# Kernel tuning notes

Hardware: AMD Instinct MI355X
Metric: run time of the kernel (lower is better)

Reference implementation:

```python
import jax, jax.numpy as jnp
import numpy as np

NUM_HEADS = 16
SOFTPLUS_EPS = 1e-4


def rotate_half(x):
    x1, x2 = jnp.split(x, 2, axis=-1)
    return jnp.concatenate((-x2, x1), axis=-1)


def setup_inputs() -> dict:
    key = jax.random.key(0)
    B, S, H = 1, 2048, 2048
    D = H // NUM_HEADS  # 128
    ks = jax.random.split(key, 5)
    hidden_states = jax.random.normal(ks[0], (B, S, H), dtype=jnp.float32)
    # standard RoPE tables: [S, D]
    inv_freq = 1.0 / (10000.0 ** (np.arange(0, D, 2, dtype=np.float32) / D))
    freqs = np.outer(np.arange(S, dtype=np.float32), inv_freq)  # [S, D/2]
    emb = np.concatenate([freqs, freqs], axis=-1)  # [S, D]
    cos = jnp.asarray(np.cos(emb), dtype=jnp.float32)
    sin = jnp.asarray(np.sin(emb), dtype=jnp.float32)
    std = 0.02
    w_q = jax.random.normal(ks[1], (2 * H, H), dtype=jnp.float32) * std
    w_k = jax.random.normal(ks[2], (2 * H, H), dtype=jnp.float32) * std
    w_v = jax.random.normal(ks[3], (H, H), dtype=jnp.float32) * std
    w_o = jax.random.normal(ks[4], (H, H), dtype=jnp.float32) * std
    return {"hidden_states": hidden_states, "cos": cos, "sin": sin,
            "w_q": w_q, "w_k": w_k, "w_v": w_v, "w_o": w_o}


def reference(hidden_states, cos, sin, w_q, w_k, w_v, w_o):
    B, S, H = hidden_states.shape
    NH = NUM_HEADS
    D = H // NH
    # projections (torch Linear: y = x @ W.T)
    q = (hidden_states @ w_q.T).reshape(B, S, NH, 2 * D).swapaxes(1, 2)  # [B,NH,S,2D]
    k = (hidden_states @ w_k.T).reshape(B, S, NH, 2 * D).swapaxes(1, 2)
    v = (hidden_states @ w_v.T).reshape(B, S, NH, D).swapaxes(1, 2)      # [B,NH,S,D]
    q_mu, q_sigma_raw = jnp.split(q, 2, axis=-1)
    k_mu, k_sigma_raw = jnp.split(k, 2, axis=-1)
    q_sigma = jax.nn.softplus(q_sigma_raw) + SOFTPLUS_EPS
    k_sigma = jax.nn.softplus(k_sigma_raw) + SOFTPLUS_EPS
    q_w = q_mu / jnp.sqrt(q_sigma)
    k_w = k_mu / jnp.sqrt(k_sigma)
    # RoPE on variance-weighted means; cos/sin [S,D] broadcast over [B,NH,S,D]
    q_w = q_w * cos + rotate_half(q_w) * sin
    k_w = k_w * cos + rotate_half(k_w) * sin
    q_sq = jnp.sum(q_w * q_w, axis=-1, keepdims=True)          # [B,NH,S,1]
    k_sq = jnp.sum(k_w * k_w, axis=-1, keepdims=True)          # [B,NH,S,1]
    dot = jnp.einsum('bhqd,bhkd->bhqk', q_w, k_w)              # [B,NH,S,S]
    weighted_dist = q_sq + jnp.swapaxes(k_sq, -2, -1) - 2.0 * dot
    log_det_q = jnp.sum(jnp.log(q_sigma), axis=-1, keepdims=True)
    log_det_k = jnp.sum(jnp.log(k_sigma), axis=-1, keepdims=True)
    log_det = log_det_q + jnp.swapaxes(log_det_k, -2, -1)
    attn_scores = -0.5 * (weighted_dist + log_det)
    attn_probs = jax.nn.softmax(attn_scores, axis=-1)
    attn_out = jnp.einsum('bhqk,bhkd->bhqd', attn_probs, v)    # [B,NH,S,D]
    attn_out = attn_out.swapaxes(1, 2).reshape(B, S, H)
    return attn_out @ w_o.T
```

## Files before the change

### kernel.cpp

```cpp
#include <hip/hip_runtime.h>
#include <stdint.h>

#define S_LEN 2048
#define HID   2048
#define NHEAD 16
#define HD    128
#define NQK   8192
#define K_HID 2048

typedef _Float16 f16x8 __attribute__((ext_vector_type(8)));
typedef float    f32x4 __attribute__((ext_vector_type(4)));

__device__ __forceinline__ unsigned short f2h(float f) {
    _Float16 h = (_Float16)f;
    union { _Float16 h; unsigned short u; } c; c.h = h;
    return c.u;
}
__device__ __forceinline__ float h2f(unsigned short b) {
    union { unsigned short u; _Float16 h; } c; c.u = b;
    return (float)c.h;
}
__device__ __forceinline__ float softplus_f(float x) {
    return (x > 20.f) ? x : log1pf(expf(x));
}
__device__ __forceinline__ unsigned pk2h(float a, float b) {
    auto w = __builtin_amdgcn_cvt_pkrtz(a, b);
    union { decltype(w) h; unsigned u; } c; c.h = w;
    return c.u;
}
#define EXP2F(x) __builtin_amdgcn_exp2f(x)
#define LOG2E 1.44269504088896f
__device__ __forceinline__ void gload_lds16(const unsigned short* g, unsigned short* l) {
    __builtin_amdgcn_global_load_lds(
        (const __attribute__((address_space(1))) unsigned int*)g,
        (__attribute__((address_space(3))) unsigned int*)l, 16, 0, 0);
}
__device__ __forceinline__ void bar() {
    asm volatile("" ::: "memory");
    __builtin_amdgcn_s_barrier();
    asm volatile("" ::: "memory");
}
#define VMCNT(n) asm volatile("s_waitcnt vmcnt(" #n ")" ::: "memory")

__global__ __launch_bounds__(256) void cast5(const float* __restrict__ hs,
                                             const float* __restrict__ wq,
                                             const float* __restrict__ wk,
                                             const float* __restrict__ wv,
                                             const float* __restrict__ wo,
                                             unsigned short* __restrict__ hs16,
                                             unsigned short* __restrict__ wqk16,
                                             unsigned short* __restrict__ wv16,
                                             unsigned short* __restrict__ wo16) {
    int b = blockIdx.x;
    const float* src;
    unsigned short* dst;
    int i;
    if (b < 4096)       { src = hs; dst = hs16;                          i = b; }
    else if (b < 12288) { src = wq; dst = wqk16;                         i = b - 4096; }
    else if (b < 20480) { src = wk; dst = wqk16 + (size_t)4096 * K_HID;  i = b - 12288; }
    else if (b < 24576) { src = wv; dst = wv16;                          i = b - 20480; }
    else                { src = wo; dst = wo16;                          i = b - 24576; }
    int idx = i * 256 + threadIdx.x;
    float4 v = ((const float4*)src)[idx];
    ushort4 o;
    o.x = f2h(v.x); o.y = f2h(v.y); o.z = f2h(v.z); o.w = f2h(v.w);
    ((ushort4*)dst)[idx] = o;
}

template <bool OUT_F16>
__device__ __forceinline__ void gemm_body(const unsigned short* __restrict__ A,
                                          const unsigned short* __restrict__ B,
                                          void* __restrict__ Cv,
                                          int m0, int n0, int N,
                                          unsigned short* As, unsigned short* Bs) {
    const int t    = threadIdx.x;
    const int wave = t >> 6;
    const int lane = t & 63;
    const int wm   = wave >> 1, wn = wave & 1;
    const int lrow = lane & 15, quad = lane >> 4;
    const int srow = lane >> 2;
    const int scol = (lane & 3) * 8;

    f32x4 acc[4][4];
    for (int i = 0; i < 4; ++i)
        for (int j = 0; j < 4; ++j)
            acc[i][j] = (f32x4){0.f, 0.f, 0.f, 0.f};

    for (int k0 = 0; k0 < K_HID; k0 += 32) {
        for (int c = 0; c < 2; ++c) {
            int ch = wave * 2 + c;
            int row = ch * 16 + srow;
            gload_lds16(A + (size_t)(m0 + row) * K_HID + k0 + scol, &As[ch * 512]);
            gload_lds16(B + (size_t)(n0 + row) * K_HID + k0 + scol, &Bs[ch * 512]);
        }
        __syncthreads();

        f16x8 af[4], bfr[4];
        for (int tm = 0; tm < 4; ++tm)
            af[tm]  = *(const f16x8*)(&As[(wm * 64 + tm * 16 + lrow) * 32 + quad * 8]);
        for (int tn = 0; tn < 4; ++tn)
            bfr[tn] = *(const f16x8*)(&Bs[(wn * 64 + tn * 16 + lrow) * 32 + quad * 8]);
        for (int tm = 0; tm < 4; ++tm)
            for (int tn = 0; tn < 4; ++tn)
                acc[tm][tn] = __builtin_amdgcn_mfma_f32_16x16x32_f16(af[tm], bfr[tn], acc[tm][tn], 0, 0, 0);
        __syncthreads();
    }

    for (int tm = 0; tm < 4; ++tm)
        for (int tn = 0; tn < 4; ++tn) {
            int col = n0 + wn * 64 + tn * 16 + lrow;
            for (int r = 0; r < 4; ++r) {
                int row = m0 + wm * 64 + tm * 16 + quad * 4 + r;
                if (OUT_F16)
                    ((unsigned short*)Cv)[(size_t)row * N + col] = f2h(acc[tm][tn][r]);
                else
                    ((float*)Cv)[(size_t)row * N + col] = acc[tm][tn][r];
            }
        }
}

__global__ __launch_bounds__(256) void gemm_qkv(const unsigned short* __restrict__ hs16,
                                                const unsigned short* __restrict__ wqk16,
                                                const unsigned short* __restrict__ wv16,
                                                unsigned short* __restrict__ qk16,
                                                unsigned short* __restrict__ Vt) {
    __shared__ __align__(16) unsigned short As[128 * 32];
    __shared__ __align__(16) unsigned short Bs[128 * 32];
    int b = blockIdx.x;
    if (b < 1024) {
        gemm_body<true>(hs16, wqk16, qk16, (b >> 6) * 128, (b & 63) * 128, NQK, As, Bs);
    } else {
        b -= 1024;
        gemm_body<true>(wv16, hs16, Vt, (b >> 4) * 128, (b & 15) * 128, S_LEN, As, Bs);
    }
}

template <bool OUT_F16>
__global__ __launch_bounds__(256) void gemm_nt_f16(const unsigned short* __restrict__ A,
                                                   const unsigned short* __restrict__ B,
                                                   void* __restrict__ Cv,
                                                   int M, int N, int Kd) {
    __shared__ __align__(16) unsigned short As[128 * 32];
    __shared__ __align__(16) unsigned short Bs[128 * 32];
    gemm_body<OUT_F16>(A, B, Cv, blockIdx.y * 128, blockIdx.x * 128, N, As, Bs);
}

__global__ __launch_bounds__(512, 2) void gemm256_qk(const unsigned short* __restrict__ A,
                                                     const unsigned short* __restrict__ B,
                                                     unsigned short* __restrict__ C) {
    extern __shared__ __align__(16) unsigned short lds[];
    const int t    = threadIdx.x;
    const int wave = t >> 6;
    const int lane = t & 63;
    const int wm   = wave >> 2, wn = wave & 3;
    const int lrow = lane & 15, quad = lane >> 4;

    const int x  = blockIdx.x & 7;
    const int sl = blockIdx.x >> 3;
    const int tm = ((x >> 2) << 2) + (sl >> 3);
    const int tn = ((x & 3) << 3) + (sl & 7);
    const int m0 = tm << 8, n0 = tn << 8;

    const int srow = lane >> 2;
    const int scol = ((lane & 3) * 8) ^ ((lane >> 5) << 4);
    const unsigned short* Ag = A + (size_t)(m0 + wave * 16 + srow) * K_HID + scol;
    const unsigned short* Bg = B + (size_t)(n0 + wave * 16 + srow) * K_HID + scol;

    const int swz = (lrow * 32 + quad * 8) ^ ((lrow >> 3) << 4);

    f32x4 acc[8][4];
    #pragma unroll
    for (int i = 0; i < 8; ++i)
        #pragma unroll
        for (int j = 0; j < 4; ++j) acc[i][j] = (f32x4){0.f, 0.f, 0.f, 0.f};

    {
        unsigned short* la = lds + wave * 1024;
        gload_lds16(Ag,               la);
        gload_lds16(Ag + 32,          la + 512);
        gload_lds16(Ag + 262144,      la + 8192);
        gload_lds16(Ag + 262144 + 32, la + 8704);
        unsigned short* lb = la + 16384;
        gload_lds16(Bg,               lb);
        gload_lds16(Bg + 32,          lb + 512);
        gload_lds16(Bg + 262144,      lb + 8192);
        gload_lds16(Bg + 262144 + 32, lb + 8704);
    }
    VMCNT(0);
    bar();

    f16x8 ah[4][2], b01[2][2];

    const int NT = K_HID / 64;
    #pragma unroll 1
    for (int t2 = 0; t2 < NT; ++t2) {
        const int buf = t2 & 1;
        const unsigned short* Lb = lds + buf * 32768;
        unsigned short*       Ln = lds + (buf ^ 1) * 32768 + wave * 1024;
        const int k1  = (t2 + 1) * 64;
        const bool pre = (t2 < NT - 1);

        f16x8 al[4][2], b23[2][2];

        if (pre) {
            gload_lds16(Ag + k1,               Ln);
            gload_lds16(Ag + k1 + 32,          Ln + 512);
            gload_lds16(Ag + 262144 + k1,      Ln + 8192);
            gload_lds16(Ag + 262144 + k1 + 32, Ln + 8704);
        }
        #pragma unroll
        for (int i = 0; i < 4; ++i) {
            al[i][0] = *(const f16x8*)(Lb + (wm * 8 + i) * 1024 + swz);
            al[i][1] = *(const f16x8*)(Lb + (wm * 8 + i) * 1024 + 512 + swz);
        }
        if (t2) {
            __builtin_amdgcn_s_setprio(1);
            #pragma unroll
            for (int i = 0; i < 4; ++i)
                #pragma unroll
                for (int j = 0; j < 2; ++j) {
                    acc[4 + i][j] = __builtin_amdgcn_mfma_f32_16x16x32_f16(ah[i][0], b01[j][0], acc[4 + i][j], 0, 0, 0);
                    acc[4 + i][j] = __builtin_amdgcn_mfma_f32_16x16x32_f16(ah[i][1], b01[j][1], acc[4 + i][j], 0, 0, 0);
                }
            __builtin_amdgcn_s_setprio(0);
        }
        #pragma unroll
        for (int j = 0; j < 2; ++j) {
            b01[j][0] = *(const f16x8*)(Lb + 16384 + (wn * 4 + j) * 1024 + swz);
            b01[j][1] = *(const f16x8*)(Lb + 16384 + (wn * 4 + j) * 1024 + 512 + swz);
        }
        bar();

        if (pre) {
            gload_lds16(Bg + k1,               Ln + 16384);
            gload_lds16(Bg + k1 + 32,          Ln + 16896);
            gload_lds16(Bg + 262144 + k1,      Ln + 24576);
            gload_lds16(Bg + 262144 + k1 + 32, Ln + 25088);
        }
        #pragma unroll
        for (int j = 0; j < 2; ++j) {
            b23[j][0] = *(const f16x8*)(Lb + 16384 + (wn * 4 + 2 + j) * 1024 + swz);
            b23[j][1] = *(const f16x8*)(Lb + 16384 + (wn * 4 + 2 + j) * 1024 + 512 + swz);
        }
        __builtin_amdgcn_s_setprio(1);
        #pragma unroll
        for (int i = 0; i < 4; ++i)
            #pragma unroll
            for (int j = 0; j < 2; ++j) {
                acc[i][j] = __builtin_amdgcn_mfma_f32_16x16x32_f16(al[i][0], b01[j][0], acc[i][j], 0, 0, 0);
                acc[i][j] = __builtin_amdgcn_mfma_f32_16x16x32_f16(al[i][1], b01[j][1], acc[i][j], 0, 0, 0);
            }
        __builtin_amdgcn_s_setprio(0);
        bar();

        #pragma unroll
        for (int i = 0; i < 4; ++i) {
            ah[i][0] = *(const f16x8*)(Lb + (wm * 8 + 4 + i) * 1024 + swz);
            ah[i][1] = *(const f16x8*)(Lb + (wm * 8 + 4 + i) * 1024 + 512 + swz);
        }
        __builtin_amdgcn_s_setprio(1);
        #pragma unroll
        for (int i = 0; i < 4; ++i)
            #pragma unroll
            for (int j = 0; j < 2; ++j) {
                acc[i][2 + j] = __builtin_amdgcn_mfma_f32_16x16x32_f16(al[i][0], b23[j][0], acc[i][2 + j], 0, 0, 0);
                acc[i][2 + j] = __builtin_amdgcn_mfma_f32_16x16x32_f16(al[i][1], b23[j][1], acc[i][2 + j], 0, 0, 0);
            }
        __builtin_amdgcn_s_setprio(0);
        bar();

        __builtin_amdgcn_s_setprio(1);
        #pragma unroll
        for (int i = 0; i < 4; ++i)
            #pragma unroll
            for (int j = 0; j < 2; ++j) {
                acc[4 + i][2 + j] = __builtin_amdgcn_mfma_f32_16x16x32_f16(ah[i][0], b23[j][0], acc[4 + i][2 + j], 0, 0, 0);
                acc[4 + i][2 + j] = __builtin_amdgcn_mfma_f32_16x16x32_f16(ah[i][1], b23[j][1], acc[4 + i][2 + j], 0, 0, 0);
            }
        __builtin_amdgcn_s_setprio(0);
        VMCNT(0);
        bar();
    }

    __builtin_amdgcn_s_setprio(1);
    #pragma unroll
    for (int i = 0; i < 4; ++i)
        #pragma unroll
        for (int j = 0; j < 2; ++j) {
            acc[4 + i][j] = __builtin_amdgcn_mfma_f32_16x16x32_f16(ah[i][0], b01[j][0], acc[4 + i][j], 0, 0, 0);
            acc[4 + i][j] = __builtin_amdgcn_mfma_f32_16x16x32_f16(ah[i][1], b01[j][1], acc[4 + i][j], 0, 0, 0);
        }
    __builtin_amdgcn_s_setprio(0);

    #pragma unroll
    for (int m = 0; m < 8; ++m)
        #pragma unroll
        for (int n = 0; n < 4; ++n) {
            const int col = n0 + wn * 64 + n * 16 + lrow;
            #pragma unroll
            for (int r = 0; r < 4; ++r) {
                const int row = m0 + wm * 128 + m * 16 + quad * 4 + r;
                C[(size_t)row * NQK + col] = f2h(acc[m][n][r]);
            }
        }
}

__global__ __launch_bounds__(256) void prep_qk(const unsigned short* __restrict__ qk,
                                               const float* __restrict__ cosb,
                                               const float* __restrict__ sinb,
                                               unsigned short* __restrict__ Q16,
                                               unsigned short* __restrict__ K16,
                                               float* __restrict__ kbias) {
    int gid  = blockIdx.x * 4 + (threadIdx.x >> 6);
    int lane = threadIdx.x & 63;
    int h = gid >> 11;
    int s = gid & 2047;
    int d1 = lane, d2 = lane + 64;
    const unsigned short* row = qk + (size_t)s * NQK;
    float c1 = cosb[s * HD + d1], c2 = cosb[s * HD + d2];
    float s1 = sinb[s * HD + d1], s2 = sinb[s * HD + d2];
    size_t ob = ((size_t)h * S_LEN + s) * HD;

    {
        int base = h * 256;
        float mu1 = h2f(row[base + d1]),       mu2 = h2f(row[base + d2]);
        float sg1 = softplus_f(h2f(row[base + 128 + d1])) + 1e-4f;
        float sg2 = softplus_f(h2f(row[base + 128 + d2])) + 1e-4f;
        float w1 = mu1 * rsqrtf(sg1), w2 = mu2 * rsqrtf(sg2);
        float o1 = w1 * c1 - w2 * s1;
        float o2 = w2 * c2 + w1 * s2;
        Q16[ob + d1] = f2h(o1 * LOG2E);
        Q16[ob + d2] = f2h(o2 * LOG2E);
    }
    {
        int base = 4096 + h * 256;
        float mu1 = h2f(row[base + d1]),       mu2 = h2f(row[base + d2]);
        float sg1 = softplus_f(h2f(row[base + 128 + d1])) + 1e-4f;
        float sg2 = softplus_f(h2f(row[base + 128 + d2])) + 1e-4f;
        float w1 = mu1 * rsqrtf(sg1), w2 = mu2 * rsqrtf(sg2);
        float o1 = w1 * c1 - w2 * s1;
        float o2 = w2 * c2 + w1 * s2;
        unsigned short k1 = f2h(o1), k2 = f2h(o2);
        K16[ob + d1] = k1; K16[ob + d2] = k2;
        float r1 = h2f(k1), r2 = h2f(k2);
        float part = r1 * r1 + r2 * r2 + logf(sg1) + logf(sg2);
        for (int off = 32; off > 0; off >>= 1) part += __shfl_down(part, off);
        if (lane == 0) kbias[(size_t)h * S_LEN + s] = -0.5f * LOG2E * part;
    }
}

__global__ __launch_bounds__(256, 2) void flash_mfma(const unsigned short* __restrict__ Q16,
                                                     const unsigned short* __restrict__ K16,
                                                     const unsigned short* __restrict__ Vt,
                                                     const float* __restrict__ kbias,
                                                     unsigned short* __restrict__ OP,
                                                     float* __restrict__ ML) {
    constexpr int LV = 72;
    __shared__ __align__(16) unsigned short Khs[4 * 64 * 32];
    __shared__ __align__(16) unsigned short Vts[2 * 128 * 32];
    __shared__ __align__(16) unsigned short Ps[128 * LV];
    __shared__ float kb[64];

    const int t    = threadIdx.x;
    const int bb   = blockIdx.x;
    const int cc   = (bb & 7) | (((bb >> 7) & 3) << 3);
    const int h    = cc & 15;
    const int kz   = cc >> 4;
    const int q0   = ((bb >> 3) & 15) * 128;
    const int wave = t >> 6;
    const int lane = t & 63;
    const int lrow = lane & 15, quad = lane >> 4;
    const int srow = lane >> 2;
    const int scol = (lane & 3) * 8;

    f16x8 qf[2][4];
    for (int m = 0; m < 2; ++m) {
        size_t rb = ((size_t)h * S_LEN + q0 + wave * 32 + m * 16 + lrow) * HD;
        for (int kk = 0; kk < 4; ++kk)
            qf[m][kk] = *(const f16x8*)(Q16 + rb + kk * 32 + quad * 8);
    }

    float mrow[2], lsum[2];
    f32x4 Ofr[2][8];
    for (int m = 0; m < 2; ++m) { mrow[m] = -INFINITY; lsum[m] = 0.f; }
    for (int m = 0; m < 2; ++m)
        for (int d = 0; d < 8; ++d) Ofr[m][d] = (f32x4){0.f, 0.f, 0.f, 0.f};

    const int kbeg = kz * 1024;
    for (int k0 = kbeg; k0 < kbeg + 1024; k0 += 64) {
        {
            const unsigned short* kgb = K16 + ((size_t)h * S_LEN + k0) * HD;
            const unsigned short* vgb = Vt + ((size_t)h * HD) * S_LEN + k0;
            for (int c = 0; c < 4; ++c) {
                int ch = wave * 4 + c;
                int kk = ch >> 2;
                int r  = (ch & 3) * 16 + srow;
                gload_lds16(kgb + (size_t)r * HD + kk * 32 + scol, &Khs[ch * 512]);
                int kc = ch >> 3;
                int r2 = (ch & 7) * 16 + srow;
                gload_lds16(vgb + (size_t)r2 * S_LEN + kc * 32 + scol, &Vts[ch * 512]);
            }
            if (t < 64) kb[t] = kbias[(size_t)h * S_LEN + k0 + t];
        }
        __syncthreads();

        f32x4 sc[2][4];
        for (int m = 0; m < 2; ++m)
            for (int nt = 0; nt < 4; ++nt) sc[m][nt] = (f32x4){0.f, 0.f, 0.f, 0.f};
        for (int kk = 0; kk < 4; ++kk)
            for (int nt = 0; nt < 4; ++nt) {
                f16x8 khf = *(const f16x8*)(&Khs[kk * 2048 + (nt * 16 + lrow) * 32 + quad * 8]);
                sc[0][nt] = __builtin_amdgcn_mfma_f32_16x16x32_f16(khf, qf[0][kk], sc[0][nt], 0, 0, 0);
                sc[1][nt] = __builtin_amdgcn_mfma_f32_16x16x32_f16(khf, qf[1][kk], sc[1][nt], 0, 0, 0);
            }

        f32x4 kbv[4];
        #pragma unroll
        for (int nt = 0; nt < 4; ++nt)
            kbv[nt] = *(const f32x4*)(&kb[nt * 16 + quad * 4]);

        #pragma unroll
        for (int m = 0; m < 2; ++m) {
            float s[4][4];
            float mx = -INFINITY;
            #pragma unroll
            for (int nt = 0; nt < 4; ++nt)
                #pragma unroll
                for (int r = 0; r < 4; ++r) {
                    s[nt][r] = sc[m][nt][r] + kbv[nt][r];
                    mx = fmaxf(mx, s[nt][r]);
                }
            mx = fmaxf(mx, __shfl_xor(mx, 16));
            mx = fmaxf(mx, __shfl_xor(mx, 32));
            float mnew  = fmaxf(mrow[m], mx);
            float alpha = EXP2F(mrow[m] - mnew);
            mrow[m] = mnew;
            float psum = 0.f;
            unsigned pw[8];
            #pragma unroll
            for (int nt = 0; nt < 4; ++nt) {
                float p0 = EXP2F(s[nt][0] - mnew);
                float p1 = EXP2F(s[nt][1] - mnew);
                float p2 = EXP2F(s[nt][2] - mnew);
                float p3 = EXP2F(s[nt][3] - mnew);
                psum += (p0 + p1) + (p2 + p3);
                pw[nt * 2]     = pk2h(p0, p1);
                pw[nt * 2 + 1] = pk2h(p2, p3);
            }
            lsum[m] = lsum[m] * alpha + psum;
            float av0 = __shfl(alpha, quad * 4 + 0);
            float av1 = __shfl(alpha, quad * 4 + 1);
            float av2 = __shfl(alpha, quad * 4 + 2);
            float av3 = __shfl(alpha, quad * 4 + 3);
            #pragma unroll
            for (int dt = 0; dt < 8; ++dt) {
                Ofr[m][dt][0] *= av0;
                Ofr[m][dt][1] *= av1;
                Ofr[m][dt][2] *= av2;
                Ofr[m][dt][3] *= av3;
            }
            int prow = (wave * 32 + m * 16 + lrow) * LV;
            #pragma unroll
            for (int nt = 0; nt < 4; ++nt) {
                uint2 wv; wv.x = pw[nt * 2]; wv.y = pw[nt * 2 + 1];
                *(uint2*)(&Ps[prow + nt * 16 + quad * 4]) = wv;
            }
        }

        for (int c = 0; c < 2; ++c) {
            f16x8 pa0 = *(const f16x8*)(&Ps[(wave * 32 + lrow) * LV + c * 32 + quad * 8]);
            f16x8 pa1 = *(const f16x8*)(&Ps[(wave * 32 + 16 + lrow) * LV + c * 32 + quad * 8]);
            for (int dt = 0; dt < 8; ++dt) {
                f16x8 vb = *(const f16x8*)(&Vts[c * 4096 + (dt * 16 + lrow) * 32 + quad * 8]);
                Ofr[0][dt] = __builtin_amdgcn_mfma_f32_16x16x32_f16(pa0, vb, Ofr[0][dt], 0, 0, 0);
                Ofr[1][dt] = __builtin_amdgcn_mfma_f32_16x16x32_f16(pa1, vb, Ofr[1][dt], 0, 0, 0);
            }
        }
        __syncthreads();
    }

    size_t obase = (size_t)(kz * NHEAD + h) * S_LEN;
    for (int m = 0; m < 2; ++m) {
        float rs = lsum[m];
        rs += __shfl_xor(rs, 16);
        rs += __shfl_xor(rs, 32);
        if (quad == 0) {
            int qrow = q0 + wave * 32 + m * 16 + lrow;
            ML[(obase + qrow) * 2]     = mrow[m];
            ML[(obase + qrow) * 2 + 1] = rs;
        }
        for (int r = 0; r < 4; ++r) {
            int qrow = q0 + wave * 32 + m * 16 + quad * 4 + r;
            unsigned short* op = OP + (obase + qrow) * HD;
            for (int dt = 0; dt < 8; ++dt)
                op[dt * 16 + lrow] = f2h(Ofr[m][dt][r]);
        }
    }
}

__global__ __launch_bounds__(256) void flash_merge(const unsigned short* __restrict__ OP,
                                                   const float* __restrict__ ML,
                                                   unsigned short* __restrict__ Obf) {
    int row = blockIdx.x * 2 + (threadIdx.x >> 7);
    int d   = threadIdx.x & 127;
    int h = row >> 11, q = row & 2047;
    size_t i0 = (size_t)h * S_LEN + q;
    size_t i1 = (size_t)(NHEAD + h) * S_LEN + q;
    float m0 = ML[i0 * 2], l0 = ML[i0 * 2 + 1];
    float m1 = ML[i1 * 2], l1 = ML[i1 * 2 + 1];
    float mf = fmaxf(m0, m1);
    float w0 = EXP2F(m0 - mf), w1 = EXP2F(m1 - mf);
    float inv = 1.f / (l0 * w0 + l1 * w1);
    float o = (h2f(OP[i0 * HD + d]) * w0 + h2f(OP[i1 * HD + d]) * w1) * inv;
    Obf[(size_t)q * HID + h * HD + d] = f2h(o);
}

extern "C" void kernel_launch(void* const* d_in, const int* in_sizes, int n_in,
                              void* d_out, int out_size, void* d_ws, size_t ws_size,
                              hipStream_t stream) {
    const float* hs   = (const float*)d_in[0];
    const float* cosb = (const float*)d_in[1];
    const float* sinb = (const float*)d_in[2];
    const float* wq   = (const float*)d_in[3];
    const float* wk   = (const float*)d_in[4];
    const float* wv   = (const float*)d_in[5];
    const float* wo   = (const float*)d_in[6];
    float* out = (float*)d_out;
    char*  ws  = (char*)d_ws;

    unsigned short* w_qk16 = (unsigned short*)(ws);
    unsigned short* Q16    = (unsigned short*)(ws);
    unsigned short* K16    = (unsigned short*)(ws + 8388608);
    float*          kbias  = (float*)(ws + 16777216);
    unsigned short* qk16   = (unsigned short*)(ws + 33554432);
    unsigned short* OP     = (unsigned short*)(ws + 33554432);
    float*          ML     = (float*)(ws + 50331648);
    unsigned short* hs16   = (unsigned short*)(ws + 67108864);
    unsigned short* Obf    = (unsigned short*)(ws + 67108864);
    unsigned short* w_v16  = (unsigned short*)(ws + 75497472);
    unsigned short* w_o16  = (unsigned short*)(ws + 83886080);
    unsigned short* Vt     = (unsigned short*)(ws + 92274688);

    static int use256 = -1;
    if (use256 < 0) {
        hipError_t e = hipFuncSetAttribute((const void*)gemm256_qk,
                                           hipFuncAttributeMaxDynamicSharedMemorySize,
                                           131072);
        use256 = (e == hipSuccess) ? 1 : 0;
    }

    cast5<<<28672, 256, 0, stream>>>(hs, wq, wk, wv, wo, hs16, w_qk16, w_v16, w_o16);

    if (use256) {
        gemm256_qk<<<256, 512, 131072, stream>>>(hs16, w_qk16, qk16);
        gemm_nt_f16<true><<<dim3(16, 16), 256, 0, stream>>>(w_v16, hs16, Vt, HID, S_LEN, K_HID);
    } else {
        gemm_qkv<<<1280, 256, 0, stream>>>(hs16, w_qk16, w_v16, qk16, Vt);
    }

    prep_qk<<<(NHEAD * S_LEN) / 4, 256, 0, stream>>>(qk16, cosb, sinb,
                                                     Q16, K16, kbias);
    flash_mfma<<<512, 256, 0, stream>>>(Q16, K16, Vt, kbias, OP, ML);
    flash_merge<<<(NHEAD * S_LEN) / 2, 256, 0, stream>>>(OP, ML, Obf);
    gemm_nt_f16<false><<<dim3(16, 16), 256, 0, stream>>>(Obf, w_o16, out, S_LEN, HID, K_HID);
}
```

Measured before the change: 379.6 us.

## Fuse V projection with QK prep kernel and skip redundant softmax rescales

The V projection GEMM and the per-row Q/K prep (softplus, RoPE, key bias) now run as one launch, with separate block ranges doing each job. This removes a kernel boundary and lets the two independent workloads share the GPU. In the flash kernel the key bias is used as the initial MFMA accumulator, which removes a separate add. The running-max rescale of the output accumulators is skipped when no lane's row maximum increases, at the cost of a wave-wide vote and a branch per step.

```diff
diff --git a/kernel.cpp b/kernel.cpp
--- a/kernel.cpp
+++ b/kernel.cpp
@@ -119,200 +119,13 @@
         }
 }
 
-__global__ __launch_bounds__(256) void gemm_qkv(const unsigned short* __restrict__ hs16,
-                                                const unsigned short* __restrict__ wqk16,
-                                                const unsigned short* __restrict__ wv16,
-                                                unsigned short* __restrict__ qk16,
-                                                unsigned short* __restrict__ Vt) {
-    __shared__ __align__(16) unsigned short As[128 * 32];
-    __shared__ __align__(16) unsigned short Bs[128 * 32];
-    int b = blockIdx.x;
-    if (b < 1024) {
-        gemm_body<true>(hs16, wqk16, qk16, (b >> 6) * 128, (b & 63) * 128, NQK, As, Bs);
-    } else {
-        b -= 1024;
-        gemm_body<true>(wv16, hs16, Vt, (b >> 4) * 128, (b & 15) * 128, S_LEN, As, Bs);
-    }
-}
-
-template <bool OUT_F16>
-__global__ __launch_bounds__(256) void gemm_nt_f16(const unsigned short* __restrict__ A,
-                                                   const unsigned short* __restrict__ B,
-                                                   void* __restrict__ Cv,
-                                                   int M, int N, int Kd) {
-    __shared__ __align__(16) unsigned short As[128 * 32];
-    __shared__ __align__(16) unsigned short Bs[128 * 32];
-    gemm_body<OUT_F16>(A, B, Cv, blockIdx.y * 128, blockIdx.x * 128, N, As, Bs);
-}
-
-__global__ __launch_bounds__(512, 2) void gemm256_qk(const unsigned short* __restrict__ A,
-                                                     const unsigned short* __restrict__ B,
-                                                     unsigned short* __restrict__ C) {
-    extern __shared__ __align__(16) unsigned short lds[];
-    const int t    = threadIdx.x;
-    const int wave = t >> 6;
-    const int lane = t & 63;
-    const int wm   = wave >> 2, wn = wave & 3;
-    const int lrow = lane & 15, quad = lane >> 4;
-
-    const int x  = blockIdx.x & 7;
-    const int sl = blockIdx.x >> 3;
-    const int tm = ((x >> 2) << 2) + (sl >> 3);
-    const int tn = ((x & 3) << 3) + (sl & 7);
-    const int m0 = tm << 8, n0 = tn << 8;
-
-    const int srow = lane >> 2;
-    const int scol = ((lane & 3) * 8) ^ ((lane >> 5) << 4);
-    const unsigned short* Ag = A + (size_t)(m0 + wave * 16 + srow) * K_HID + scol;
-    const unsigned short* Bg = B + (size_t)(n0 + wave * 16 + srow) * K_HID + scol;
-
-    const int swz = (lrow * 32 + quad * 8) ^ ((lrow >> 3) << 4);
-
-    f32x4 acc[8][4];
-    #pragma unroll
-    for (int i = 0; i < 8; ++i)
-        #pragma unroll
-        for (int j = 0; j < 4; ++j) acc[i][j] = (f32x4){0.f, 0.f, 0.f, 0.f};
-
-    {
-        unsigned short* la = lds + wave * 1024;
-        gload_lds16(Ag,               la);
-        gload_lds16(Ag + 32,          la + 512);
-        gload_lds16(Ag + 262144,      la + 8192);
-        gload_lds16(Ag + 262144 + 32, la + 8704);
-        unsigned short* lb = la + 16384;
-        gload_lds16(Bg,               lb);
-        gload_lds16(Bg + 32,          lb + 512);
-        gload_lds16(Bg + 262144,      lb + 8192);
-        gload_lds16(Bg + 262144 + 32, lb + 8704);
-    }
-    VMCNT(0);
-    bar();
-
-    f16x8 ah[4][2], b01[2][2];
-
-    const int NT = K_HID / 64;
-    #pragma unroll 1
-    for (int t2 = 0; t2 < NT; ++t2) {
-        const int buf = t2 & 1;
-        const unsigned short* Lb = lds + buf * 32768;
-        unsigned short*       Ln = lds + (buf ^ 1) * 32768 + wave * 1024;
-        const int k1  = (t2 + 1) * 64;
-        const bool pre = (t2 < NT - 1);
-
-        f16x8 al[4][2], b23[2][2];
-
-        if (pre) {
-            gload_lds16(Ag + k1,               Ln);
-            gload_lds16(Ag + k1 + 32,          Ln + 512);
-            gload_lds16(Ag + 262144 + k1,      Ln + 8192);
-            gload_lds16(Ag + 262144 + k1 + 32, Ln + 8704);
-        }
-        #pragma unroll
-        for (int i = 0; i < 4; ++i) {
-            al[i][0] = *(const f16x8*)(Lb + (wm * 8 + i) * 1024 + swz);
-            al[i][1] = *(const f16x8*)(Lb + (wm * 8 + i) * 1024 + 512 + swz);
-        }
-        if (t2) {
-            __builtin_amdgcn_s_setprio(1);
-            #pragma unroll
-            for (int i = 0; i < 4; ++i)
-                #pragma unroll
-                for (int j = 0; j < 2; ++j) {
-                    acc[4 + i][j] = __builtin_amdgcn_mfma_f32_16x16x32_f16(ah[i][0], b01[j][0], acc[4 + i][j], 0, 0, 0);
-                    acc[4 + i][j] = __builtin_amdgcn_mfma_f32_16x16x32_f16(ah[i][1], b01[j][1], acc[4 + i][j], 0, 0, 0);
-                }
-            __builtin_amdgcn_s_setprio(0);
-        }
-        #pragma unroll
-        for (int j = 0; j < 2; ++j) {
-            b01[j][0] = *(const f16x8*)(Lb + 16384 + (wn * 4 + j) * 1024 + swz);
-            b01[j][1] = *(const f16x8*)(Lb + 16384 + (wn * 4 + j) * 1024 + 512 + swz);
-        }
-        bar();
-
-        if (pre) {
-            gload_lds16(Bg + k1,               Ln + 16384);
-            gload_lds16(Bg + k1 + 32,          Ln + 16896);
-            gload_lds16(Bg + 262144 + k1,      Ln + 24576);
-            gload_lds16(Bg + 262144 + k1 + 32, Ln + 25088);
-        }
-        #pragma unroll
-        for (int j = 0; j < 2; ++j) {
-            b23[j][0] = *(const f16x8*)(Lb + 16384 + (wn * 4 + 2 + j) * 1024 + swz);
-            b23[j][1] = *(const f16x8*)(Lb + 16384 + (wn * 4 + 2 + j) * 1024 + 512 + swz);
-        }
-        __builtin_amdgcn_s_setprio(1);
-        #pragma unroll
-        for (int i = 0; i < 4; ++i)
-            #pragma unroll
-            for (int j = 0; j < 2; ++j) {
-                acc[i][j] = __builtin_amdgcn_mfma_f32_16x16x32_f16(al[i][0], b01[j][0], acc[i][j], 0, 0, 0);
-                acc[i][j] = __builtin_amdgcn_mfma_f32_16x16x32_f16(al[i][1], b01[j][1], acc[i][j], 0, 0, 0);
-            }
-        __builtin_amdgcn_s_setprio(0);
-        bar();
-
-        #pragma unroll
-        for (int i = 0; i < 4; ++i) {
-            ah[i][0] = *(const f16x8*)(Lb + (wm * 8 + 4 + i) * 1024 + swz);
-            ah[i][1] = *(const f16x8*)(Lb + (wm * 8 + 4 + i) * 1024 + 512 + swz);
-        }
-        __builtin_amdgcn_s_setprio(1);
-        #pragma unroll
-        for (int i = 0; i < 4; ++i)
-            #pragma unroll
-            for (int j = 0; j < 2; ++j) {
-                acc[i][2 + j] = __builtin_amdgcn_mfma_f32_16x16x32_f16(al[i][0], b23[j][0], acc[i][2 + j], 0, 0, 0);
-                acc[i][2 + j] = __builtin_amdgcn_mfma_f32_16x16x32_f16(al[i][1], b23[j][1], acc[i][2 + j], 0, 0, 0);
-            }
-        __builtin_amdgcn_s_setprio(0);
-        bar();
-
-        __builtin_amdgcn_s_setprio(1);
-        #pragma unroll
-        for (int i = 0; i < 4; ++i)
-            #pragma unroll
-            for (int j = 0; j < 2; ++j) {
-                acc[4 + i][2 + j] = __builtin_amdgcn_mfma_f32_16x16x32_f16(ah[i][0], b23[j][0], acc[4 + i][2 + j], 0, 0, 0);
-                acc[4 + i][2 + j] = __builtin_amdgcn_mfma_f32_16x16x32_f16(ah[i][1], b23[j][1], acc[4 + i][2 + j], 0, 0, 0);
-            }
-        __builtin_amdgcn_s_setprio(0);
-        VMCNT(0);
-        bar();
-    }
-
-    __builtin_amdgcn_s_setprio(1);
-    #pragma unroll
-    for (int i = 0; i < 4; ++i)
-        #pragma unroll
-        for (int j = 0; j < 2; ++j) {
-            acc[4 + i][j] = __builtin_amdgcn_mfma_f32_16x16x32_f16(ah[i][0], b01[j][0], acc[4 + i][j], 0, 0, 0);
-            acc[4 + i][j] = __builtin_amdgcn_mfma_f32_16x16x32_f16(ah[i][1], b01[j][1], acc[4 + i][j], 0, 0, 0);
-        }
-    __builtin_amdgcn_s_setprio(0);
-
-    #pragma unroll
-    for (int m = 0; m < 8; ++m)
-        #pragma unroll
-        for (int n = 0; n < 4; ++n) {
-            const int col = n0 + wn * 64 + n * 16 + lrow;
-            #pragma unroll
-            for (int r = 0; r < 4; ++r) {
-                const int row = m0 + wm * 128 + m * 16 + quad * 4 + r;
-                C[(size_t)row * NQK + col] = f2h(acc[m][n][r]);
-            }
-        }
-}
-
-__global__ __launch_bounds__(256) void prep_qk(const unsigned short* __restrict__ qk,
-                                               const float* __restrict__ cosb,
-                                               const float* __restrict__ sinb,
-                                               unsigned short* __restrict__ Q16,
-                                               unsigned short* __restrict__ K16,
-                                               float* __restrict__ kbias) {
-    int gid  = blockIdx.x * 4 + (threadIdx.x >> 6);
-    int lane = threadIdx.x & 63;
+__device__ __forceinline__ void prep_body(int gid, int lane,
+                                          const unsigned short* __restrict__ qk,
+                                          const float* __restrict__ cosb,
+                                          const float* __restrict__ sinb,
+                                          unsigned short* __restrict__ Q16,
+                                          unsigned short* __restrict__ K16,
+                                          float* __restrict__ kbias) {
     int h = gid >> 11;
     int s = gid & 2047;
     int d1 = lane, d2 = lane + 64;
@@ -349,6 +162,222 @@
     }
 }
 
+__global__ __launch_bounds__(256) void gemm_qkv(const unsigned short* __restrict__ hs16,
+                                                const unsigned short* __restrict__ wqk16,
+                                                const unsigned short* __restrict__ wv16,
+                                                unsigned short* __restrict__ qk16,
+                                                unsigned short* __restrict__ Vt) {
+    __shared__ __align__(16) unsigned short As[128 * 32];
+    __shared__ __align__(16) unsigned short Bs[128 * 32];
+    int b = blockIdx.x;
+    if (b < 1024) {
+        gemm_body<true>(hs16, wqk16, qk16, (b >> 6) * 128, (b & 63) * 128, NQK, As, Bs);
+    } else {
+        b -= 1024;
+        gemm_body<true>(wv16, hs16, Vt, (b >> 4) * 128, (b & 15) * 128, S_LEN, As, Bs);
+    }
+}
+
+template <bool OUT_F16>
+__global__ __launch_bounds__(256) void gemm_nt_f16(const unsigned short* __restrict__ A,
+                                                   const unsigned short* __restrict__ B,
+                                                   void* __restrict__ Cv,
+                                                   int M, int N, int Kd) {
+    __shared__ __align__(16) unsigned short As[128 * 32];
+    __shared__ __align__(16) unsigned short Bs[128 * 32];
+    gemm_body<OUT_F16>(A, B, Cv, blockIdx.y * 128, blockIdx.x * 128, N, As, Bs);
+}
+
+__global__ __launch_bounds__(256) void vt_prep(const unsigned short* __restrict__ wv16,
+                                               const unsigned short* __restrict__ hs16,
+                                               unsigned short* __restrict__ Vt,
+                                               const unsigned short* __restrict__ qk16,
+                                               const float* __restrict__ cosb,
+                                               const float* __restrict__ sinb,
+                                               unsigned short* __restrict__ Q16,
+                                               unsigned short* __restrict__ K16,
+                                               float* __restrict__ kbias) {
+    __shared__ __align__(16) unsigned short As[128 * 32];
+    __shared__ __align__(16) unsigned short Bs[128 * 32];
+    int b = blockIdx.x;
+    if (b < 256) {
+        gemm_body<true>(wv16, hs16, Vt, (b >> 4) * 128, (b & 15) * 128, S_LEN, As, Bs);
+    } else {
+        int gid = (b - 256) * 4 + (threadIdx.x >> 6);
+        prep_body(gid, threadIdx.x & 63, qk16, cosb, sinb, Q16, K16, kbias);
+    }
+}
+
+__global__ __launch_bounds__(256) void prep_qk(const unsigned short* __restrict__ qk,
+                                               const float* __restrict__ cosb,
+                                               const float* __restrict__ sinb,
+                                               unsigned short* __restrict__ Q16,
+                                               unsigned short* __restrict__ K16,
+                                               float* __restrict__ kbias) {
+    int gid = blockIdx.x * 4 + (threadIdx.x >> 6);
+    prep_body(gid, threadIdx.x & 63, qk, cosb, sinb, Q16, K16, kbias);
+}
+
+__global__ __launch_bounds__(512, 2) void gemm256_qk(const unsigned short* __restrict__ A,
+                                                     const unsigned short* __restrict__ B,
+                                                     unsigned short* __restrict__ C) {
+    extern __shared__ __align__(16) unsigned short lds[];
+    const int t    = threadIdx.x;
+    const int wave = t >> 6;
+    const int lane = t & 63;
+    const int wm   = wave >> 2, wn = wave & 3;
+    const int lrow = lane & 15, quad = lane >> 4;
+
+    const int x  = blockIdx.x & 7;
+    const int sl = blockIdx.x >> 3;
+    const int tm = ((x >> 2) << 2) + (sl >> 3);
+    const int tn = ((x & 3) << 3) + (sl & 7);
+    const int m0 = tm << 8, n0 = tn << 8;
+
+    const int srow = lane >> 2;
+    const int scol = ((lane & 3) * 8) ^ ((lane >> 5) << 4);
+    const unsigned short* Ag = A + (size_t)(m0 + wave * 16 + srow) * K_HID + scol;
+    const unsigned short* Bg = B + (size_t)(n0 + wave * 16 + srow) * K_HID + scol;
+
+    const int swz = (lrow * 32 + quad * 8) ^ ((lrow >> 3) << 4);
+
+    f32x4 acc[8][4];
+    #pragma unroll
+    for (int i = 0; i < 8; ++i)
+        #pragma unroll
+        for (int j = 0; j < 4; ++j) acc[i][j] = (f32x4){0.f, 0.f, 0.f, 0.f};
+
+    {
+        unsigned short* la = lds + wave * 1024;
+        gload_lds16(Ag,               la);
+        gload_lds16(Ag + 32,          la + 512);
+        gload_lds16(Ag + 262144,      la + 8192);
+        gload_lds16(Ag + 262144 + 32, la + 8704);
+        unsigned short* lb = la + 16384;
+        gload_lds16(Bg,               lb);
+        gload_lds16(Bg + 32,          lb + 512);
+        gload_lds16(Bg + 262144,      lb + 8192);
+        gload_lds16(Bg + 262144 + 32, lb + 8704);
+    }
+    VMCNT(0);
+    bar();
+
+    f16x8 ah[4][2], b01[2][2];
+
+    const int NT = K_HID / 64;
+    #pragma unroll 1
+    for (int t2 = 0; t2 < NT; ++t2) {
+        const int buf = t2 & 1;
+        const unsigned short* Lb = lds + buf * 32768;
+        unsigned short*       Ln = lds + (buf ^ 1) * 32768 + wave * 1024;
+        const int k1  = (t2 + 1) * 64;
+        const bool pre = (t2 < NT - 1);
+
+        f16x8 al[4][2], b23[2][2];
+
+        if (pre) {
+            gload_lds16(Ag + k1,               Ln);
+            gload_lds16(Ag + k1 + 32,          Ln + 512);
+            gload_lds16(Ag + 262144 + k1,      Ln + 8192);
+            gload_lds16(Ag + 262144 + k1 + 32, Ln + 8704);
+        }
+        #pragma unroll
+        for (int i = 0; i < 4; ++i) {
+            al[i][0] = *(const f16x8*)(Lb + (wm * 8 + i) * 1024 + swz);
+            al[i][1] = *(const f16x8*)(Lb + (wm * 8 + i) * 1024 + 512 + swz);
+        }
+        if (t2) {
+            __builtin_amdgcn_s_setprio(1);
+            #pragma unroll
+            for (int i = 0; i < 4; ++i)
+                #pragma unroll
+                for (int j = 0; j < 2; ++j) {
+                    acc[4 + i][j] = __builtin_amdgcn_mfma_f32_16x16x32_f16(ah[i][0], b01[j][0], acc[4 + i][j], 0, 0, 0);
+                    acc[4 + i][j] = __builtin_amdgcn_mfma_f32_16x16x32_f16(ah[i][1], b01[j][1], acc[4 + i][j], 0, 0, 0);
+                }
+            __builtin_amdgcn_s_setprio(0);
+        }
+        #pragma unroll
+        for (int j = 0; j < 2; ++j) {
+            b01[j][0] = *(const f16x8*)(Lb + 16384 + (wn * 4 + j) * 1024 + swz);
+            b01[j][1] = *(const f16x8*)(Lb + 16384 + (wn * 4 + j) * 1024 + 512 + swz);
+        }
+        bar();
+
+        if (pre) {
+            gload_lds16(Bg + k1,               Ln + 16384);
+            gload_lds16(Bg + k1 + 32,          Ln + 16896);
+            gload_lds16(Bg + 262144 + k1,      Ln + 24576);
+            gload_lds16(Bg + 262144 + k1 + 32, Ln + 25088);
+        }
+        #pragma unroll
+        for (int j = 0; j < 2; ++j) {
+            b23[j][0] = *(const f16x8*)(Lb + 16384 + (wn * 4 + 2 + j) * 1024 + swz);
+            b23[j][1] = *(const f16x8*)(Lb + 16384 + (wn * 4 + 2 + j) * 1024 + 512 + swz);
+        }
+        __builtin_amdgcn_s_setprio(1);
+        #pragma unroll
+        for (int i = 0; i < 4; ++i)
+            #pragma unroll
+            for (int j = 0; j < 2; ++j) {
+                acc[i][j] = __builtin_amdgcn_mfma_f32_16x16x32_f16(al[i][0], b01[j][0], acc[i][j], 0, 0, 0);
+                acc[i][j] = __builtin_amdgcn_mfma_f32_16x16x32_f16(al[i][1], b01[j][1], acc[i][j], 0, 0, 0);
+            }
+        __builtin_amdgcn_s_setprio(0);
+        bar();
+
+        #pragma unroll
+        for (int i = 0; i < 4; ++i) {
+            ah[i][0] = *(const f16x8*)(Lb + (wm * 8 + 4 + i) * 1024 + swz);
+            ah[i][1] = *(const f16x8*)(Lb + (wm * 8 + 4 + i) * 1024 + 512 + swz);
+        }
+        __builtin_amdgcn_s_setprio(1);
+        #pragma unroll
+        for (int i = 0; i < 4; ++i)
+            #pragma unroll
+            for (int j = 0; j < 2; ++j) {
+                acc[i][2 + j] = __builtin_amdgcn_mfma_f32_16x16x32_f16(al[i][0], b23[j][0], acc[i][2 + j], 0, 0, 0);
+                acc[i][2 + j] = __builtin_amdgcn_mfma_f32_16x16x32_f16(al[i][1], b23[j][1], acc[i][2 + j], 0, 0, 0);
+            }
+        __builtin_amdgcn_s_setprio(0);
+        bar();
+
+        __builtin_amdgcn_s_setprio(1);
+        #pragma unroll
+        for (int i = 0; i < 4; ++i)
+            #pragma unroll
+            for (int j = 0; j < 2; ++j) {
+                acc[4 + i][2 + j] = __builtin_amdgcn_mfma_f32_16x16x32_f16(ah[i][0], b23[j][0], acc[4 + i][2 + j], 0, 0, 0);
+                acc[4 + i][2 + j] = __builtin_amdgcn_mfma_f32_16x16x32_f16(ah[i][1], b23[j][1], acc[4 + i][2 + j], 0, 0, 0);
+            }
+        __builtin_amdgcn_s_setprio(0);
+        VMCNT(0);
+        bar();
+    }
+
+    __builtin_amdgcn_s_setprio(1);
+    #pragma unroll
+    for (int i = 0; i < 4; ++i)
+        #pragma unroll
+        for (int j = 0; j < 2; ++j) {
+            acc[4 + i][j] = __builtin_amdgcn_mfma_f32_16x16x32_f16(ah[i][0], b01[j][0], acc[4 + i][j], 0, 0, 0);
+            acc[4 + i][j] = __builtin_amdgcn_mfma_f32_16x16x32_f16(ah[i][1], b01[j][1], acc[4 + i][j], 0, 0, 0);
+        }
+    __builtin_amdgcn_s_setprio(0);
+
+    #pragma unroll
+    for (int m = 0; m < 8; ++m)
+        #pragma unroll
+        for (int n = 0; n < 4; ++n) {
+            const int col = n0 + wn * 64 + n * 16 + lrow;
+            #pragma unroll
+            for (int r = 0; r < 4; ++r) {
+                const int row = m0 + wm * 128 + m * 16 + quad * 4 + r;
+                C[(size_t)row * NQK + col] = f2h(acc[m][n][r]);
+            }
+        }
+}
+
 __global__ __launch_bounds__(256, 2) void flash_mfma(const unsigned short* __restrict__ Q16,
                                                      const unsigned short* __restrict__ K16,
                                                      const unsigned short* __restrict__ Vt,
@@ -404,9 +433,16 @@
         }
         __syncthreads();
 
+        f32x4 kbv[4];
+        #pragma unroll
+        for (int nt = 0; nt < 4; ++nt)
+            kbv[nt] = *(const f32x4*)(&kb[nt * 16 + quad * 4]);
+
         f32x4 sc[2][4];
+        #pragma unroll
         for (int m = 0; m < 2; ++m)
-            for (int nt = 0; nt < 4; ++nt) sc[m][nt] = (f32x4){0.f, 0.f, 0.f, 0.f};
+            #pragma unroll
+            for (int nt = 0; nt < 4; ++nt) sc[m][nt] = kbv[nt];
         for (int kk = 0; kk < 4; ++kk)
             for (int nt = 0; nt < 4; ++nt) {
                 f16x8 khf = *(const f16x8*)(&Khs[kk * 2048 + (nt * 16 + lrow) * 32 + quad * 8]);
@@ -414,51 +450,46 @@
                 sc[1][nt] = __builtin_amdgcn_mfma_f32_16x16x32_f16(khf, qf[1][kk], sc[1][nt], 0, 0, 0);
             }
 
-        f32x4 kbv[4];
-        #pragma unroll
-        for (int nt = 0; nt < 4; ++nt)
-            kbv[nt] = *(const f32x4*)(&kb[nt * 16 + quad * 4]);
-
         #pragma unroll
         for (int m = 0; m < 2; ++m) {
-            float s[4][4];
             float mx = -INFINITY;
             #pragma unroll
             for (int nt = 0; nt < 4; ++nt)
                 #pragma unroll
-                for (int r = 0; r < 4; ++r) {
-                    s[nt][r] = sc[m][nt][r] + kbv[nt][r];
-                    mx = fmaxf(mx, s[nt][r]);
-                }
+                for (int r = 0; r < 4; ++r)
+                    mx = fmaxf(mx, sc[m][nt][r]);
             mx = fmaxf(mx, __shfl_xor(mx, 16));
             mx = fmaxf(mx, __shfl_xor(mx, 32));
-            float mnew  = fmaxf(mrow[m], mx);
-            float alpha = EXP2F(mrow[m] - mnew);
-            mrow[m] = mnew;
+            if (!__all(mx <= mrow[m])) {
+                float mnew  = fmaxf(mrow[m], mx);
+                float alpha = EXP2F(mrow[m] - mnew);
+                mrow[m] = mnew;
+                lsum[m] *= alpha;
+                float av0 = __shfl(alpha, quad * 4 + 0);
+                float av1 = __shfl(alpha, quad * 4 + 1);
+                float av2 = __shfl(alpha, quad * 4 + 2);
+                float av3 = __shfl(alpha, quad * 4 + 3);
+                #pragma unroll
+                for (int dt = 0; dt < 8; ++dt) {
+                    Ofr[m][dt][0] *= av0;
+                    Ofr[m][dt][1] *= av1;
+                    Ofr[m][dt][2] *= av2;
+                    Ofr[m][dt][3] *= av3;
+                }
+            }
             float psum = 0.f;
             unsigned pw[8];
             #pragma unroll
             for (int nt = 0; nt < 4; ++nt) {
-                float p0 = EXP2F(s[nt][0] - mnew);
-                float p1 = EXP2F(s[nt][1] - mnew);
-                float p2 = EXP2F(s[nt][2] - mnew);
-                float p3 = EXP2F(s[nt][3] - mnew);
+                float p0 = EXP2F(sc[m][nt][0] - mrow[m]);
+                float p1 = EXP2F(sc[m][nt][1] - mrow[m]);
+                float p2 = EXP2F(sc[m][nt][2] - mrow[m]);
+                float p3 = EXP2F(sc[m][nt][3] - mrow[m]);
                 psum += (p0 + p1) + (p2 + p3);
                 pw[nt * 2]     = pk2h(p0, p1);
                 pw[nt * 2 + 1] = pk2h(p2, p3);
             }
-            lsum[m] = lsum[m] * alpha + psum;
-            float av0 = __shfl(alpha, quad * 4 + 0);
-            float av1 = __shfl(alpha, quad * 4 + 1);
-            float av2 = __shfl(alpha, quad * 4 + 2);
-            float av3 = __shfl(alpha, quad * 4 + 3);
-            #pragma unroll
-            for (int dt = 0; dt < 8; ++dt) {
-                Ofr[m][dt][0] *= av0;
-                Ofr[m][dt][1] *= av1;
-                Ofr[m][dt][2] *= av2;
-                Ofr[m][dt][3] *= av3;
-            }
+            lsum[m] += psum;
             int prow = (wave * 32 + m * 16 + lrow) * LV;
             #pragma unroll
             for (int nt = 0; nt < 4; ++nt) {
@@ -553,13 +584,14 @@
 
     if (use256) {
         gemm256_qk<<<256, 512, 131072, stream>>>(hs16, w_qk16, qk16);
-        gemm_nt_f16<true><<<dim3(16, 16), 256, 0, stream>>>(w_v16, hs16, Vt, HID, S_LEN, K_HID);
+        vt_prep<<<256 + 8192, 256, 0, stream>>>(w_v16, hs16, Vt, qk16,
+                                                cosb, sinb, Q16, K16, kbias);
     } else {
         gemm_qkv<<<1280, 256, 0, stream>>>(hs16, w_qk16, w_v16, qk16, Vt);
-    }
-
-    prep_qk<<<(NHEAD * S_LEN) / 4, 256, 0, stream>>>(qk16, cosb, sinb,
-                                                     Q16, K16, kbias);
+        prep_qk<<<(NHEAD * S_LEN) / 4, 256, 0, stream>>>(qk16, cosb, sinb,
+                                                         Q16, K16, kbias);
+    }
+
     flash_mfma<<<512, 256, 0, stream>>>(Q16, K16, Vt, kbias, OP, ML);
     flash_merge<<<(NHEAD * S_LEN) / 2, 256, 0, stream>>>(OP, ML, Obf);
     gemm_nt_f16<false><<<dim3(16, 16), 256, 0, stream>>>(Obf, w_o16, out, S_LEN, HID, K_HID);
```

Measured after the change: 369.9 us (median of 3 runs). 1.03x faster.
